# Optimization experiments

Hardware: AMD Instinct MI355X
Metric: run time of the kernel (lower is better)

Reference implementation:

```python
import jax, jax.numpy as jnp
import numpy as np

# Kornia's fixed 5x5 pyramid (binomial) kernel used by build_pyramid/pyrdown
_PYR_K = np.array([[1, 4, 6, 4, 1],
                   [4, 16, 24, 16, 4],
                   [6, 24, 36, 24, 6],
                   [4, 16, 24, 16, 4],
                   [1, 4, 6, 4, 1]], dtype=np.float32) / 256.0


def _pyrdown(x):
    """kornia pyrdown: 5x5 binomial blur (reflect pad) + bilinear resize to (H//2, W//2)."""
    B, C, H, W = x.shape
    xp = jnp.pad(x, ((0, 0), (0, 0), (2, 2), (2, 2)), mode='reflect')
    k = jnp.broadcast_to(jnp.asarray(_PYR_K, x.dtype), (C, 1, 5, 5))  # depthwise
    y = jax.lax.conv_general_dilated(
        xp, k, window_strides=(1, 1), padding='VALID',
        feature_group_count=C, dimension_numbers=('NCHW', 'OIHW', 'NCHW'))
    # torch F.interpolate bilinear align_corners=False == jax resize bilinear, antialias off
    return jax.image.resize(y, (B, C, H // 2, W // 2), method='bilinear', antialias=False)


def _norm_pc(x):
    """Per-channel min-max normalization to [0,1] over spatial dims."""
    mx = jnp.max(x, axis=(2, 3), keepdims=True)
    mn = jnp.min(x, axis=(2, 3), keepdims=True)
    return (x - mn) / (mx - mn)


def _avg_local_max(x):
    """Mean of 16x16 tile maxima; torch loop range(0, H-16, 16) skips the last tile
    row/col, and with zero tiles the torch code yields nan_to_num(0/0) == 0."""
    B, C, H, W = x.shape
    s = 16
    ny = len(range(0, H - s, s))
    nx = len(range(0, W - s, s))
    if ny == 0 or nx == 0:
        return jnp.zeros((B, C, 1, 1), x.dtype)
    t = x[:, :, :ny * s, :nx * s].reshape(B, C, ny, s, nx, s)
    lmax = jnp.max(t, axis=(3, 5))           # [B,C,ny,nx]
    return jnp.mean(lmax, axis=(2, 3)).reshape(B, C, 1, 1)


def _sm_normalization(x):
    d = _norm_pc(x)
    lm = _avg_local_max(d)
    return d * (1.0 - lm) ** 2


def setup_inputs() -> dict:
    key = jax.random.key(0)
    x = jax.random.normal(key, (8, 3, 512, 512), dtype=jnp.float32)
    return {"x": x}


def reference(x):
    B, C, H, W = x.shape
    inp = _norm_pc(x)
    max_level = int(H).bit_length() - 1   # 9 for H=512
    u = max_level - 1

    # Gaussian pyramid of length max_level: [inp, pyrdown(inp), ...]
    pyr = [inp]
    for _ in range(max_level - 1):
        pyr.append(_pyrdown(pyr[-1]))

    acc = None
    for i in range(u - 1):
        h, w = pyr[i + 1].shape[2], pyr[i + 1].shape[3]
        up = jnp.repeat(jnp.repeat(pyr[i + 2], 2, axis=2), 2, axis=3)[:, :, :h, :w]
        d = jnp.abs(pyr[i + 1] - up)
        nd = jax.image.resize(_sm_normalization(d), (B, C, H, W),
                              method='bilinear', antialias=False)
        acc = nd if acc is None else acc + nd

    return jnp.mean(acc, axis=1)  # [B,H,W]
```

## Files before the change

kernel.cpp:

```cpp
#include <hip/hip_runtime.h>
#include <math.h>

#define NPLANES 24
#define FINF 3.402823466e38f

__host__ __device__ __forceinline__ int d_off(int li) {
    return 2097152 - (2097152 >> (2 * li));
}

__device__ __forceinline__ int refl(int v, int S) {
    if (v < 0) v = -v;
    if (v >= S) v = 2 * S - 2 - v;
    return v;
}

__device__ __forceinline__ void wminmax64(float& mn, float& mx) {
#pragma unroll
    for (int o = 32; o > 0; o >>= 1) {
        mn = fminf(mn, __shfl_xor(mn, o, 64));
        mx = fmaxf(mx, __shfl_xor(mx, o, 64));
    }
}
__device__ __forceinline__ float wsumx64(float v) {
#pragma unroll
    for (int o = 32; o > 0; o >>= 1) v += __shfl_xor(v, o, 64);
    return v;
}
__device__ __forceinline__ void wminmax16(float& mn, float& mx) {
#pragma unroll
    for (int o = 8; o > 0; o >>= 1) {
        mn = fminf(mn, __shfl_xor(mn, o, 16));
        mx = fmaxf(mx, __shfl_xor(mx, o, 16));
    }
}

__device__ __forceinline__ float stencil6(const float* s, int S, int i, int j) {
    const float w[6] = {1.f, 5.f, 10.f, 10.f, 5.f, 1.f};
    int rx[6];
#pragma unroll
    for (int b = 0; b < 6; ++b) rx[b] = refl(2 * j - 2 + b, S);
    float acc = 0.f;
#pragma unroll
    for (int a = 0; a < 6; ++a) {
        int ry = refl(2 * i - 2 + a, S);
        const float* rp = s + ry * S;
        float r = 0.f;
#pragma unroll
        for (int b = 0; b < 6; ++b) r += w[b] * rp[rx[b]];
        acc += w[a] * r;
    }
    return acc * (1.f / 1024.f);
}

__global__ __launch_bounds__(256) void pyrdown_l1(const float* __restrict__ in,
                                                  float* __restrict__ out) {
    constexpr int IS = 512, SO = 256, TO = 32, TI = 68, TPA = 8;
    __shared__ float sIn[TI * TI];
    __shared__ float sH[TI * TO];
    const int tid = threadIdx.x;
    const int p = blockIdx.x / (TPA * TPA);
    const int t = blockIdx.x % (TPA * TPA);
    const int ty = t / TPA, tx = t % TPA;
    const int oy = ty * TO, ox = tx * TO;
    const int iy = 2 * oy - 2, ix = 2 * ox - 2;
    const float* ip = in + (size_t)p * IS * IS;

    for (int k = tid; k < TI * TI; k += 256) {
        int r = k / TI, c = k - r * TI;
        sIn[k] = ip[refl(iy + r, IS) * IS + refl(ix + c, IS)];
    }
    __syncthreads();
    for (int k = tid; k < TI * 8; k += 256) {
        int r = k >> 3, jq = k & 7;
        const float4* rp = (const float4*)(sIn + r * TI + 8 * jq);
        float4 v0 = rp[0], v1 = rp[1], v2 = rp[2];
        float4 o;
        o.x = v0.x + 5.f * v0.y + 10.f * v0.z + 10.f * v0.w + 5.f * v1.x + v1.y;
        o.y = v0.z + 5.f * v0.w + 10.f * v1.x + 10.f * v1.y + 5.f * v1.z + v1.w;
        o.z = v1.x + 5.f * v1.y + 10.f * v1.z + 10.f * v1.w + 5.f * v2.x + v2.y;
        o.w = v1.z + 5.f * v1.w + 10.f * v2.x + 10.f * v2.y + 5.f * v2.z + v2.w;
        *(float4*)(sH + r * TO + 4 * jq) = o;
    }
    __syncthreads();
    {
        int i = tid >> 3, jq = tid & 7;
        const float* base = sH + (2 * i) * TO + 4 * jq;
        float4 r0 = *(const float4*)(base);
        float4 r1 = *(const float4*)(base + TO);
        float4 r2 = *(const float4*)(base + 2 * TO);
        float4 r3 = *(const float4*)(base + 3 * TO);
        float4 r4 = *(const float4*)(base + 4 * TO);
        float4 r5 = *(const float4*)(base + 5 * TO);
        float4 o;
        o.x = (r0.x + 5.f * r1.x + 10.f * r2.x + 10.f * r3.x + 5.f * r4.x + r5.x) * (1.f / 1024.f);
        o.y = (r0.y + 5.f * r1.y + 10.f * r2.y + 10.f * r3.y + 5.f * r4.y + r5.y) * (1.f / 1024.f);
        o.z = (r0.z + 5.f * r1.z + 10.f * r2.z + 10.f * r3.z + 5.f * r4.z + r5.z) * (1.f / 1024.f);
        o.w = (r0.w + 5.f * r1.w + 10.f * r2.w + 10.f * r3.w + 5.f * r4.w + r5.w) * (1.f / 1024.f);
        *(float4*)(out + (size_t)p * SO * SO + (size_t)(oy + i) * SO + ox + 4 * jq) = o;
    }
}

__global__ __launch_bounds__(256) void pyrdown23(const float* __restrict__ pyr1,
                                                 float* __restrict__ pyr3,
                                                 float* __restrict__ dBase,
                                                 float* __restrict__ tmin0,
                                                 float* __restrict__ tmax0,
                                                 float* __restrict__ tmin1,
                                                 float* __restrict__ tmax1) {
    __shared__ float sIn[5776];
    __shared__ float sH1[2736];
    __shared__ float sP2[1296];
    __shared__ float sH2[576];
    __shared__ float sP3t[256];
    const int tid = threadIdx.x;
    const int p = blockIdx.x >> 4;
    const int t = blockIdx.x & 15;
    const int t3y = t >> 2, t3x = t & 3;
    const int oy3 = t3y * 16, ox3 = t3x * 16;
    const int oy2 = 2 * oy3, ox2 = 2 * ox3;
    const int py0 = oy2 - 2, px0 = ox2 - 2;
    const int iy0 = 2 * py0 - 2, ix0 = 2 * px0 - 2;
    const float* ip = pyr1 + (size_t)p * 65536;

    for (int k = tid; k < 5776; k += 256) {
        int r = k / 76, c = k - r * 76;
        sIn[k] = ip[refl(iy0 + r, 256) * 256 + refl(ix0 + c, 256)];
    }
    __syncthreads();
    for (int k = tid; k < 2736; k += 256) {
        int r = k / 36, c2 = k - r * 36;
        const float* rp = sIn + r * 76 + 2 * c2;
        sH1[k] = rp[0] + 5.f * rp[1] + 10.f * rp[2] + 10.f * rp[3] + 5.f * rp[4] + rp[5];
    }
    __syncthreads();
    for (int k = tid; k < 1296; k += 256) {
        int r2 = k / 36, c2 = k - r2 * 36;
        const float* cp = sH1 + 2 * r2 * 36 + c2;
        sP2[k] = (cp[0] + 5.f * cp[36] + 10.f * cp[72] + 10.f * cp[108] +
                  5.f * cp[144] + cp[180]) * (1.f / 1024.f);
    }
    __syncthreads();
    for (int k = tid; k < 576; k += 256) {
        int r2 = k >> 4, c3 = k & 15;
        int gb = 2 * (ox3 + c3) - 2;
        const float* rp = sP2 + r2 * 36;
        sH2[k] = rp[refl(gb, 128) - px0] + 5.f * rp[refl(gb + 1, 128) - px0] +
                 10.f * rp[refl(gb + 2, 128) - px0] + 10.f * rp[refl(gb + 3, 128) - px0] +
                 5.f * rp[refl(gb + 4, 128) - px0] + rp[refl(gb + 5, 128) - px0];
    }
    __syncthreads();
    {
        int i3 = tid >> 4, c3 = tid & 15;
        int gb = 2 * (oy3 + i3) - 2;
        float s = sH2[(refl(gb, 128) - py0) * 16 + c3] +
                  5.f * sH2[(refl(gb + 1, 128) - py0) * 16 + c3] +
                  10.f * sH2[(refl(gb + 2, 128) - py0) * 16 + c3] +
                  10.f * sH2[(refl(gb + 3, 128) - py0) * 16 + c3] +
                  5.f * sH2[(refl(gb + 4, 128) - py0) * 16 + c3] +
                  sH2[(refl(gb + 5, 128) - py0) * 16 + c3];
        float v = s * (1.f / 1024.f);
        sP3t[tid] = v;
        pyr3[(size_t)p * 4096 + (size_t)(oy3 + i3) * 64 + ox3 + c3] = v;
    }
    __syncthreads();
    {
        float* d0g = dBase + (size_t)p * 65536;
        int ti = tid >> 4, si = tid & 15;
        int tr = ti >> 2, tc = ti & 3;
        int y0 = tr * 16 + (si >> 2) * 4, x0 = tc * 16 + (si & 3) * 4;
        float mn = FINF, mx = -FINF;
#pragma unroll
        for (int r = 0; r < 4; ++r) {
            int y = y0 + r;
            const float* srow = sIn + (y + 6) * 76 + x0 + 6;
            const float* prow = sP2 + ((y >> 1) + 2) * 36 + 2 + (x0 >> 1);
            float e0 = prow[0], e1 = prow[1];
            float4 dv;
            dv.x = fabsf(srow[0] - e0);
            dv.y = fabsf(srow[1] - e0);
            dv.z = fabsf(srow[2] - e1);
            dv.w = fabsf(srow[3] - e1);
            *(float4*)(d0g + (size_t)(4 * oy3 + y) * 256 + 4 * ox3 + x0) = dv;
            mn = fminf(mn, fminf(fminf(dv.x, dv.y), fminf(dv.z, dv.w)));
            mx = fmaxf(mx, fmaxf(fmaxf(dv.x, dv.y), fmaxf(dv.z, dv.w)));
        }
        wminmax16(mn, mx);
        if (si == 0) {
            int g0 = p * 256 + (t3y * 4 + tr) * 16 + (t3x * 4 + tc);
            tmin0[g0] = mn;
            tmax0[g0] = mx;
        }
    }
    if (tid < 64) {
        float* d1g = dBase + d_off(1) + (size_t)p * 16384;
        int ti = tid >> 4, si = tid & 15;
        int tr = ti >> 1, tc = ti & 1;
        int y0 = tr * 16 + (si >> 2) * 4, x0 = tc * 16 + (si & 3) * 4;
        float mn = FINF, mx = -FINF;
#pragma unroll
        for (int r = 0; r < 4; ++r) {
            int y = y0 + r;
            const float* prow = sP2 + (y + 2) * 36 + 2 + x0;
            const float* qrow = sP3t + (y >> 1) * 16 + (x0 >> 1);
            float e0 = qrow[0], e1 = qrow[1];
            float4 dv;
            dv.x = fabsf(prow[0] - e0);
            dv.y = fabsf(prow[1] - e0);
            dv.z = fabsf(prow[2] - e1);
            dv.w = fabsf(prow[3] - e1);
            *(float4*)(d1g + (size_t)(oy2 + y) * 128 + ox2 + x0) = dv;
            mn = fminf(mn, fminf(fminf(dv.x, dv.y), fminf(dv.z, dv.w)));
            mx = fmaxf(mx, fmaxf(fmaxf(dv.x, dv.y), fmaxf(dv.z, dv.w)));
        }
        wminmax16(mn, mx);
        if (si == 0) {
            int g1 = p * 64 + (t3y * 2 + tr) * 8 + (t3x * 2 + tc);
            tmin1[g1] = mn;
            tmax1[g1] = mx;
        }
    }
}

__global__ __launch_bounds__(1024) void fused_small_kernel(const float* __restrict__ pyr3,
                                                           float* __restrict__ dBase,
                                                           const float* __restrict__ tmin0,
                                                           const float* __restrict__ tmax0,
                                                           const float* __restrict__ tmin1,
                                                           const float* __restrict__ tmax1,
                                                           float* __restrict__ A,
                                                           float* __restrict__ B) {
    __shared__ float sP3[4096];
    __shared__ float sd2[4096];
    __shared__ float sp4[1024], sd3[1024];
    __shared__ float sp5[256], sd4[256];
    __shared__ float sp6[64], sd5[64];
    __shared__ float sp7[16], sd6[16];
    const int tid = threadIdx.x;
    const int p = blockIdx.x;

    if (tid < 1024) ((float4*)sP3)[tid] = ((const float4*)(pyr3 + (size_t)p * 4096))[tid];
    __syncthreads();
    {
        float* d2g = dBase + d_off(2) + (size_t)p * 4096;
        int i = tid >> 5, j = tid & 31;
        float v = stencil6(sP3, 64, i, j);
        sp4[tid] = v;
#pragma unroll
        for (int di = 0; di < 2; ++di)
#pragma unroll
            for (int dj = 0; dj < 2; ++dj) {
                int y = 2 * i + di, x = 2 * j + dj;
                float dv = fabsf(sP3[y * 64 + x] - v);
                sd2[y * 64 + x] = dv;
                d2g[y * 64 + x] = dv;
            }
    }
    __syncthreads();

    const int wave = tid >> 6, lane = tid & 63;

    if (wave == 0) {
        float* d3g = dBase + d_off(3) + (size_t)p * 1024;
#pragma unroll
        for (int q = 0; q < 4; ++q) {
            int k = lane + 64 * q;
            int i = k >> 4, j = k & 15;
            float v = stencil6(sp4, 32, i, j);
            sp5[k] = v;
#pragma unroll
            for (int di = 0; di < 2; ++di)
#pragma unroll
                for (int dj = 0; dj < 2; ++dj) {
                    int y = 2 * i + di, x = 2 * j + dj;
                    float dv = fabsf(sp4[y * 32 + x] - v);
                    sd3[y * 32 + x] = dv;
                    d3g[y * 32 + x] = dv;
                }
        }
        {
            int i = lane >> 3, j = lane & 7;
            float v = stencil6(sp5, 16, i, j);
            sp6[lane] = v;
            float* d4g = dBase + d_off(4) + (size_t)p * 256;
#pragma unroll
            for (int di = 0; di < 2; ++di)
#pragma unroll
                for (int dj = 0; dj < 2; ++dj) {
                    int y = 2 * i + di, x = 2 * j + dj;
                    float dv = fabsf(sp5[y * 16 + x] - v);
                    sd4[y * 16 + x] = dv;
                    d4g[y * 16 + x] = dv;
                }
        }
        if (lane < 16) {
            int i = lane >> 2, j = lane & 3;
            float v = stencil6(sp6, 8, i, j);
            sp7[lane] = v;
            float* d5g = dBase + d_off(5) + (size_t)p * 64;
#pragma unroll
            for (int di = 0; di < 2; ++di)
#pragma unroll
                for (int dj = 0; dj < 2; ++dj) {
                    int y = 2 * i + di, x = 2 * j + dj;
                    float dv = fabsf(sp6[y * 8 + x] - v);
                    sd5[y * 8 + x] = dv;
                    d5g[y * 8 + x] = dv;
                }
        }
        if (lane < 4) {
            int i = lane >> 1, j = lane & 1;
            float v = stencil6(sp7, 4, i, j);
            float* d6g = dBase + d_off(6) + (size_t)p * 16;
#pragma unroll
            for (int di = 0; di < 2; ++di)
#pragma unroll
                for (int dj = 0; dj < 2; ++dj) {
                    int y = 2 * i + di, x = 2 * j + dj;
                    float dv = fabsf(sp7[y * 4 + x] - v);
                    sd6[y * 4 + x] = dv;
                    d6g[y * 4 + x] = dv;
                }
        }
    } else if (wave == 1) {
        float tmn = tmin1[p * 64 + lane];
        float tmx = tmax1[p * 64 + lane];
        float mn = tmn, mx = tmx;
        wminmax64(mn, mx);
        float su = ((lane >> 3) < 7 && (lane & 7) < 7) ? tmx : 0.f;
        float sum = wsumx64(su);
        if (lane == 0) {
            float inv = 1.f / (mx - mn);
            float lm = (sum * (1.f / 49.f) - mn) * inv;
            float g = (1.f - lm) * (1.f - lm);
            A[1 * NPLANES + p] = g * inv;
            B[1 * NPLANES + p] = -mn * g * inv;
        }
    } else if (wave == 2) {
        float mn = FINF, mx = -FINF, su = 0.f;
#pragma unroll
        for (int q = 0; q < 4; ++q) {
            int t = lane + 64 * q;
            float tmn = tmin0[p * 256 + t];
            float tmx = tmax0[p * 256 + t];
            mn = fminf(mn, tmn);
            mx = fmaxf(mx, tmx);
            if ((t >> 4) < 15 && (t & 15) < 15) su += tmx;
        }
        wminmax64(mn, mx);
        float sum = wsumx64(su);
        if (lane == 0) {
            float inv = 1.f / (mx - mn);
            float lm = (sum * (1.f / 225.f) - mn) * inv;
            float g = (1.f - lm) * (1.f - lm);
            A[0 * NPLANES + p] = g * inv;
            B[0 * NPLANES + p] = -mn * g * inv;
        }
    }
    __syncthreads();

    if (wave == 0) {
        const float4* sv = (const float4*)sd2;
        float mn = FINF, mx = -FINF;
#pragma unroll
        for (int q = 0; q < 16; ++q) {
            float4 v = sv[lane + 64 * q];
            mn = fminf(mn, fminf(fminf(v.x, v.y), fminf(v.z, v.w)));
            mx = fmaxf(mx, fmaxf(fmaxf(v.x, v.y), fmaxf(v.z, v.w)));
        }
        wminmax64(mn, mx);
        float tmax = -FINF;
        if (lane < 36) {
            int t = lane >> 2, r4 = lane & 3;
            int tr = t / 3, tc = t % 3;
#pragma unroll
            for (int rr = 0; rr < 4; ++rr) {
                const float4* base = (const float4*)(sd2 + (16 * tr + 4 * r4 + rr) * 64 + 16 * tc);
#pragma unroll
                for (int c = 0; c < 4; ++c) {
                    float4 v = base[c];
                    tmax = fmaxf(tmax, fmaxf(fmaxf(v.x, v.y), fmaxf(v.z, v.w)));
                }
            }
        }
        tmax = fmaxf(tmax, __shfl_xor(tmax, 1, 64));
        tmax = fmaxf(tmax, __shfl_xor(tmax, 2, 64));
        float val = ((lane & 3) == 0 && lane < 36) ? tmax : 0.f;
        float s = wsumx64(val);
        if (lane == 0) {
            float inv = 1.f / (mx - mn);
            float lm = (s * (1.f / 9.f) - mn) * inv;
            float g = (1.f - lm) * (1.f - lm);
            A[2 * NPLANES + p] = g * inv;
            B[2 * NPLANES + p] = -mn * g * inv;
        }
    } else if (wave == 1) {
        const float4* sv = (const float4*)sd3;
        float mn = FINF, mx = -FINF;
#pragma unroll
        for (int q = 0; q < 4; ++q) {
            float4 v = sv[lane + 64 * q];
            mn = fminf(mn, fminf(fminf(v.x, v.y), fminf(v.z, v.w)));
            mx = fmaxf(mx, fmaxf(fmaxf(v.x, v.y), fmaxf(v.z, v.w)));
        }
        wminmax64(mn, mx);
        float4 e4 = sv[(lane >> 2) * 8 + (lane & 3)];
        float e = fmaxf(fmaxf(e4.x, e4.y), fmaxf(e4.z, e4.w));
        float tn = e, tm = e;
        wminmax64(tn, tm);
        if (lane == 0) {
            float inv = 1.f / (mx - mn);
            float lm = (tm - mn) * inv;
            float g = (1.f - lm) * (1.f - lm);
            A[3 * NPLANES + p] = g * inv;
            B[3 * NPLANES + p] = -mn * g * inv;
        }
    } else if (wave == 2) {
        float4 v = ((const float4*)sd4)[lane];
        float mn = fminf(fminf(v.x, v.y), fminf(v.z, v.w));
        float mx = fmaxf(fmaxf(v.x, v.y), fmaxf(v.z, v.w));
        wminmax64(mn, mx);
        if (lane == 0) {
            float inv = 1.f / (mx - mn);
            A[4 * NPLANES + p] = inv; B[4 * NPLANES + p] = -mn * inv;
        }
    } else if (wave == 3) {
        float v = sd5[lane];
        float mn = v, mx = v;
        wminmax64(mn, mx);
        if (lane == 0) {
            float inv = 1.f / (mx - mn);
            A[5 * NPLANES + p] = inv; B[5 * NPLANES + p] = -mn * inv;
        }
    } else if (wave == 4) {
        float v = (lane < 16) ? sd6[lane] : sd6[0];
        float mn = v, mx = v;
        wminmax64(mn, mx);
        if (lane == 0) {
            float inv = 1.f / (mx - mn);
            A[6 * NPLANES + p] = inv; B[6 * NPLANES + p] = -mn * inv;
        }
    }
}

__global__ __launch_bounds__(256) void final_kernel(const float* __restrict__ dBase,
                                                    const float* __restrict__ A,
                                                    const float* __restrict__ Bc,
                                                    float* __restrict__ out) {
    __shared__ float patch[1700];
    __shared__ float sBtot;
    const int tid = threadIdx.x;
    const int b = blockIdx.x >> 6;
    const int tile = blockIdx.x & 63;
    const int yb = (tile >> 3) << 6;
    const int xb = (tile & 7) << 6;

    if (tid == 0) {
        float s = 0.f;
        for (int k = 0; k < 7; ++k)
            for (int c = 0; c < 3; ++c) s += Bc[k * NPLANES + b * 3 + c];
        sBtot = s;
    }

    const int dims[7] = {34, 18, 10, 6, 4, 3, 3};
    const int lofs[7] = {0, 1156, 1480, 1580, 1616, 1632, 1641};
    int baseY[7], baseX[7];
#pragma unroll
    for (int li = 0; li < 7; ++li) {
        const int S = 256 >> li;
        const float s = 1.f / (float)(2 << li);
        baseY[li] = (int)floorf((yb + 0.5f) * s - 0.5f);
        baseX[li] = (int)floorf((xb + 0.5f) * s - 0.5f);
        const int dim = dims[li];
        const int n = dim * dim;
        const float* d0p = dBase + d_off(li) + (size_t)(b * 3) * S * S;
        const float* d1p = d0p + S * S;
        const float* d2p = d1p + S * S;
        const float A0 = A[li * NPLANES + b * 3 + 0];
        const float A1 = A[li * NPLANES + b * 3 + 1];
        const float A2 = A[li * NPLANES + b * 3 + 2];
        for (int k = tid; k < n; k += 256) {
            int r = k / dim, c = k - r * dim;
            int sr = min(max(baseY[li] + r, 0), S - 1);
            int sc = min(max(baseX[li] + c, 0), S - 1);
            int si = sr * S + sc;
            patch[lofs[li] + k] = A0 * d0p[si] + A1 * d1p[si] + A2 * d2p[si];
        }
    }
    __syncthreads();

    const int ty = tid >> 4, tx = tid & 15;
    const int gy0 = yb + (ty << 2), gx0 = xb + (tx << 2);
    float acc[4][4];
#pragma unroll
    for (int i = 0; i < 4; ++i)
#pragma unroll
        for (int j = 0; j < 4; ++j) acc[i][j] = 0.f;

    {
        const int dim = 34;
        float wy[4], wx[4];
        int ry[4], cx[4];
#pragma unroll
        for (int k = 0; k < 4; ++k) {
            float fy = (gy0 + k + 0.5f) * 0.5f - 0.5f;
            float fl = floorf(fy);
            wy[k] = fy - fl; ry[k] = (int)fl - baseY[0];
            float fx = (gx0 + k + 0.5f) * 0.5f - 0.5f;
            fl = floorf(fx);
            wx[k] = fx - fl; cx[k] = (int)fl - baseX[0];
        }
        const int r0 = ry[0], c0 = cx[0];
        const float* pp = patch + r0 * dim + c0;
        float P[4][4];
#pragma unroll
        for (int r = 0; r < 4; ++r)
#pragma unroll
            for (int c = 0; c < 4; ++c) P[r][c] = pp[r * dim + c];
        float h[4][4];
#pragma unroll
        for (int j = 0; j < 4; ++j) {
            int dx = cx[j] - c0;
#pragma unroll
            for (int r = 0; r < 4; ++r) {
                float a = dx == 0 ? P[r][0] : (dx == 1 ? P[r][1] : P[r][2]);
                float bb = dx == 0 ? P[r][1] : (dx == 1 ? P[r][2] : P[r][3]);
                h[r][j] = a + wx[j] * (bb - a);
            }
        }
#pragma unroll
        for (int i = 0; i < 4; ++i) {
            int dy = ry[i] - r0;
#pragma unroll
            for (int j = 0; j < 4; ++j) {
                float h0 = dy == 0 ? h[0][j] : (dy == 1 ? h[1][j] : h[2][j]);
                float h1 = dy == 0 ? h[1][j] : (dy == 1 ? h[2][j] : h[3][j]);
                acc[i][j] += h0 + wy[i] * (h1 - h0);
            }
        }
    }
#pragma unroll
    for (int li = 1; li < 7; ++li) {
        const int dim = dims[li];
        const float* P0 = patch + lofs[li];
        const float s = 1.f / (float)(2 << li);
        float wy[4], wx[4];
        int ry[4], cx[4];
#pragma unroll
        for (int k = 0; k < 4; ++k) {
            float fy = (gy0 + k + 0.5f) * s - 0.5f;
            float fl = floorf(fy);
            wy[k] = fy - fl; ry[k] = (int)fl - baseY[li];
            float fx = (gx0 + k + 0.5f) * s - 0.5f;
            fl = floorf(fx);
            wx[k] = fx - fl; cx[k] = (int)fl - baseX[li];
        }
        const int r0 = ry[0], c0 = cx[0];
        const float* pp = P0 + r0 * dim + c0;
        float P[3][3];
#pragma unroll
        for (int r = 0; r < 3; ++r)
#pragma unroll
            for (int c = 0; c < 3; ++c) P[r][c] = pp[r * dim + c];
        float h[3][4];
#pragma unroll
        for (int j = 0; j < 4; ++j) {
            int dx = cx[j] - c0;
#pragma unroll
            for (int r = 0; r < 3; ++r) {
                float a = dx == 0 ? P[r][0] : P[r][1];
                float bb = dx == 0 ? P[r][1] : P[r][2];
                h[r][j] = a + wx[j] * (bb - a);
            }
        }
#pragma unroll
        for (int i = 0; i < 4; ++i) {
            int dy = ry[i] - r0;
#pragma unroll
            for (int j = 0; j < 4; ++j) {
                float h0 = dy == 0 ? h[0][j] : h[1][j];
                float h1 = dy == 0 ? h[1][j] : h[2][j];
                acc[i][j] += h0 + wy[i] * (h1 - h0);
            }
        }
    }

    const float bt = sBtot;
    float* op = out + ((size_t)b * 512 + gy0) * 512 + gx0;
#pragma unroll
    for (int i = 0; i < 4; ++i) {
        float4 v;
        v.x = (acc[i][0] + bt) * (1.f / 3.f);
        v.y = (acc[i][1] + bt) * (1.f / 3.f);
        v.z = (acc[i][2] + bt) * (1.f / 3.f);
        v.w = (acc[i][3] + bt) * (1.f / 3.f);
        *(float4*)(op + (size_t)i * 512) = v;
    }
}

extern "C" void kernel_launch(void* const* d_in, const int* in_sizes, int n_in,
                              void* d_out, int out_size, void* d_ws, size_t ws_size,
                              hipStream_t stream) {
    (void)in_sizes; (void)n_in; (void)out_size; (void)ws_size;
    const float* x = (const float*)d_in[0];
    float* ws = (float*)d_ws;
    float* out = (float*)d_out;

    float* pyr1 = ws;
    float* pyr3 = ws + 1572864;
    float* dBase = ws + 1671168;
    float* tmin0 = ws + 3768192;
    float* tmax0 = ws + 3774336;
    float* tmin1 = ws + 3780480;
    float* tmax1 = ws + 3782016;
    float* A = ws + 3783552;
    float* Bc = ws + 3783720;

    pyrdown_l1<<<NPLANES * 64, 256, 0, stream>>>(x, pyr1);
    pyrdown23<<<NPLANES * 16, 256, 0, stream>>>(pyr1, pyr3, dBase, tmin0, tmax0, tmin1, tmax1);
    fused_small_kernel<<<NPLANES, 1024, 0, stream>>>(pyr3, dBase, tmin0, tmax0, tmin1, tmax1, A, Bc);
    final_kernel<<<8 * 64, 256, 0, stream>>>(dBase, A, Bc, out);
}
```

Before: 103.9 us.

## Fuse small-level kernel into pyrdown23 via last-block-per-plane atomic counter

Removes the separate fused_small_kernel launch by having the last of the 16 tile blocks per plane (detected with an atomic counter plus thread fences) run the small-pyramid levels and per-plane statistics in the pyrdown23 block, reusing its shared memory. The work is remapped from 1024 threads to 256 threads with loops and reordered wave assignments. This saves one kernel launch and its dependency gap, but adds a memset launch and runs the tail work with fewer threads per plane.

```diff
diff --git a/kernel.cpp b/kernel.cpp
--- a/kernel.cpp
+++ b/kernel.cpp
@@ -106,12 +106,17 @@
                                                  float* __restrict__ tmin0,
                                                  float* __restrict__ tmax0,
                                                  float* __restrict__ tmin1,
-                                                 float* __restrict__ tmax1) {
-    __shared__ float sIn[5776];
-    __shared__ float sH1[2736];
-    __shared__ float sP2[1296];
-    __shared__ float sH2[576];
-    __shared__ float sP3t[256];
+                                                 float* __restrict__ tmax1,
+                                                 float* __restrict__ A,
+                                                 float* __restrict__ B,
+                                                 int* __restrict__ ctr) {
+    __shared__ float smem[10912];
+    __shared__ int sLast;
+    float* sIn  = smem;
+    float* sH1  = smem + 5776;
+    float* sP2  = smem + 8512;
+    float* sH2  = smem + 9808;
+    float* sP3t = smem + 10384;
     const int tid = threadIdx.x;
     const int p = blockIdx.x >> 4;
     const int t = blockIdx.x & 15;
@@ -219,46 +224,50 @@
             tmax1[g1] = mx;
         }
     }
-}
-
-__global__ __launch_bounds__(1024) void fused_small_kernel(const float* __restrict__ pyr3,
-                                                           float* __restrict__ dBase,
-                                                           const float* __restrict__ tmin0,
-                                                           const float* __restrict__ tmax0,
-                                                           const float* __restrict__ tmin1,
-                                                           const float* __restrict__ tmax1,
-                                                           float* __restrict__ A,
-                                                           float* __restrict__ B) {
-    __shared__ float sP3[4096];
-    __shared__ float sd2[4096];
-    __shared__ float sp4[1024], sd3[1024];
-    __shared__ float sp5[256], sd4[256];
-    __shared__ float sp6[64], sd5[64];
-    __shared__ float sp7[16], sd6[16];
-    const int tid = threadIdx.x;
-    const int p = blockIdx.x;
-
-    if (tid < 1024) ((float4*)sP3)[tid] = ((const float4*)(pyr3 + (size_t)p * 4096))[tid];
+
+    __syncthreads();
+    __threadfence();
+    if (tid == 0) sLast = (atomicAdd(&ctr[p], 1) == 15);
+    __syncthreads();
+    if (!sLast) return;
+    __threadfence();
+
+    float* sP3 = smem;
+    float* sd2 = smem + 4096;
+    float* sp4 = smem + 8192;
+    float* sd3 = smem + 9216;
+    float* sp5 = smem + 10240;
+    float* sd4 = smem + 10496;
+    float* sp6 = smem + 10752;
+    float* sd5 = smem + 10816;
+    float* sp7 = smem + 10880;
+    float* sd6 = smem + 10896;
+
+    for (int k = tid; k < 1024; k += 256)
+        ((float4*)sP3)[k] = ((const float4*)(pyr3 + (size_t)p * 4096))[k];
     __syncthreads();
     {
         float* d2g = dBase + d_off(2) + (size_t)p * 4096;
-        int i = tid >> 5, j = tid & 31;
-        float v = stencil6(sP3, 64, i, j);
-        sp4[tid] = v;
-#pragma unroll
-        for (int di = 0; di < 2; ++di)
-#pragma unroll
-            for (int dj = 0; dj < 2; ++dj) {
-                int y = 2 * i + di, x = 2 * j + dj;
-                float dv = fabsf(sP3[y * 64 + x] - v);
-                sd2[y * 64 + x] = dv;
-                d2g[y * 64 + x] = dv;
-            }
+#pragma unroll
+        for (int q = 0; q < 4; ++q) {
+            int k = tid + 256 * q;
+            int i = k >> 5, j = k & 31;
+            float v = stencil6(sP3, 64, i, j);
+            sp4[k] = v;
+#pragma unroll
+            for (int di = 0; di < 2; ++di)
+#pragma unroll
+                for (int dj = 0; dj < 2; ++dj) {
+                    int y = 2 * i + di, x = 2 * j + dj;
+                    float dv = fabsf(sP3[y * 64 + x] - v);
+                    sd2[y * 64 + x] = dv;
+                    d2g[y * 64 + x] = dv;
+                }
+        }
     }
     __syncthreads();
 
     const int wave = tid >> 6, lane = tid & 63;
-
     if (wave == 0) {
         float* d3g = dBase + d_off(3) + (size_t)p * 1024;
 #pragma unroll
@@ -339,12 +348,12 @@
         float mn = FINF, mx = -FINF, su = 0.f;
 #pragma unroll
         for (int q = 0; q < 4; ++q) {
-            int t = lane + 64 * q;
-            float tmn = tmin0[p * 256 + t];
-            float tmx = tmax0[p * 256 + t];
+            int tt = lane + 64 * q;
+            float tmn = tmin0[p * 256 + tt];
+            float tmx = tmax0[p * 256 + tt];
             mn = fminf(mn, tmn);
             mx = fmaxf(mx, tmx);
-            if ((t >> 4) < 15 && (t & 15) < 15) su += tmx;
+            if ((tt >> 4) < 15 && (tt & 15) < 15) su += tmx;
         }
         wminmax64(mn, mx);
         float sum = wsumx64(su);
@@ -355,10 +364,7 @@
             A[0 * NPLANES + p] = g * inv;
             B[0 * NPLANES + p] = -mn * g * inv;
         }
-    }
-    __syncthreads();
-
-    if (wave == 0) {
+    } else {
         const float4* sv = (const float4*)sd2;
         float mn = FINF, mx = -FINF;
 #pragma unroll
@@ -370,8 +376,8 @@
         wminmax64(mn, mx);
         float tmax = -FINF;
         if (lane < 36) {
-            int t = lane >> 2, r4 = lane & 3;
-            int tr = t / 3, tc = t % 3;
+            int tt = lane >> 2, r4 = lane & 3;
+            int tr = tt / 3, tc = tt % 3;
 #pragma unroll
             for (int rr = 0; rr < 4; ++rr) {
                 const float4* base = (const float4*)(sd2 + (16 * tr + 4 * r4 + rr) * 64 + 16 * tc);
@@ -393,7 +399,10 @@
             A[2 * NPLANES + p] = g * inv;
             B[2 * NPLANES + p] = -mn * g * inv;
         }
-    } else if (wave == 1) {
+    }
+    __syncthreads();
+
+    if (wave == 0) {
         const float4* sv = (const float4*)sd3;
         float mn = FINF, mx = -FINF;
 #pragma unroll
@@ -414,7 +423,7 @@
             A[3 * NPLANES + p] = g * inv;
             B[3 * NPLANES + p] = -mn * g * inv;
         }
-    } else if (wave == 2) {
+    } else if (wave == 1) {
         float4 v = ((const float4*)sd4)[lane];
         float mn = fminf(fminf(v.x, v.y), fminf(v.z, v.w));
         float mx = fmaxf(fmaxf(v.x, v.y), fmaxf(v.z, v.w));
@@ -423,7 +432,7 @@
             float inv = 1.f / (mx - mn);
             A[4 * NPLANES + p] = inv; B[4 * NPLANES + p] = -mn * inv;
         }
-    } else if (wave == 3) {
+    } else if (wave == 2) {
         float v = sd5[lane];
         float mn = v, mx = v;
         wminmax64(mn, mx);
@@ -431,7 +440,7 @@
             float inv = 1.f / (mx - mn);
             A[5 * NPLANES + p] = inv; B[5 * NPLANES + p] = -mn * inv;
         }
-    } else if (wave == 4) {
+    } else {
         float v = (lane < 16) ? sd6[lane] : sd6[0];
         float mn = v, mx = v;
         wminmax64(mn, mx);
@@ -614,9 +623,11 @@
     float* tmax1 = ws + 3782016;
     float* A = ws + 3783552;
     float* Bc = ws + 3783720;
-
+    int* ctr = (int*)(ws + 3783888);
+
+    hipMemsetAsync(ctr, 0, NPLANES * sizeof(int), stream);
     pyrdown_l1<<<NPLANES * 64, 256, 0, stream>>>(x, pyr1);
-    pyrdown23<<<NPLANES * 16, 256, 0, stream>>>(pyr1, pyr3, dBase, tmin0, tmax0, tmin1, tmax1);
-    fused_small_kernel<<<NPLANES, 1024, 0, stream>>>(pyr3, dBase, tmin0, tmax0, tmin1, tmax1, A, Bc);
+    pyrdown23<<<NPLANES * 16, 256, 0, stream>>>(pyr1, pyr3, dBase, tmin0, tmax0,
+                                                tmin1, tmax1, A, Bc, ctr);
     final_kernel<<<8 * 64, 256, 0, stream>>>(dBase, A, Bc, out);
 }
```

After: 152.5 us. 46.7% more time.
